# Kernel tuning notes

Measured on AMD Instinct MI355X. Metric: run time of the kernel, lower is better.

## Reference

```python
import jax, jax.numpy as jnp
import numpy as np

NUM_ELEC = 128
TIME_STEPS = 128  # must equal NUM_ELEC for the original module's matmuls to be shape-consistent
NUM_VOXELS = 2052
HIDDEN = 64
DCT_DIM = 512
BATCH = 64
RHO = 0.5
TAU = 0.1
PLV_THRESH = 0.5


def dct_matrix(N, K):
    n = np.arange(N)[None, :]
    k = np.arange(K)[:, None]
    m = np.sqrt(2.0 / N) * np.cos(np.pi * (2 * n + 1) * k / (2 * N))
    m[0, :] = 1.0 / np.sqrt(N)
    return jnp.asarray(m, dtype=jnp.float32)


def setup_inputs() -> dict:
    ks = jax.random.split(jax.random.key(0), 12)
    H = HIDDEN
    return {
        "z": jax.random.normal(ks[0], (BATCH, NUM_ELEC, TIME_STEPS), dtype=jnp.float32),
        "lead_field": jax.random.normal(ks[1], (NUM_VOXELS, NUM_ELEC), dtype=jnp.float32),
        "gumbel_u": jax.random.uniform(ks[2], (NUM_ELEC, NUM_ELEC), dtype=jnp.float32, minval=1e-6, maxval=1.0 - 1e-6),
        "w_gae": jax.random.normal(ks[3], (NUM_ELEC, H), dtype=jnp.float32) / np.sqrt(NUM_ELEC),
        "b_gae": jnp.zeros((H,), dtype=jnp.float32),
        "w1": jax.random.normal(ks[4], (NUM_ELEC, H), dtype=jnp.float32) / np.sqrt(NUM_ELEC),
        "b1": jnp.zeros((H,), dtype=jnp.float32),
        "w2": jax.random.normal(ks[5], (H, H), dtype=jnp.float32) / np.sqrt(H),
        "b2": jnp.zeros((H,), dtype=jnp.float32),
        "w_ih": jax.random.normal(ks[6], (3 * H, H), dtype=jnp.float32) / np.sqrt(H),
        "w_hh": jax.random.normal(ks[7], (3 * H, H), dtype=jnp.float32) / np.sqrt(H),
        "b_ih": jnp.zeros((3 * H,), dtype=jnp.float32),
        "b_hh": jnp.zeros((3 * H,), dtype=jnp.float32),
    }


def _hilbert_phases(z):
    # FFT-based analytic signal along last axis (== scipy.signal.hilbert), then instantaneous phase
    T = z.shape[-1]
    idx = jnp.arange(T)
    hf = jnp.where(idx == 0, 1.0, jnp.where(idx < T // 2, 2.0, jnp.where(idx == T // 2, 1.0, 0.0)))
    analytic = jnp.fft.ifft(jnp.fft.fft(z, axis=-1) * hf, axis=-1)
    return jnp.angle(analytic)


def _forward(z, lead_field, gumbel_u, w_gae, b_gae, w1, b1, w2, b2, w_ih, w_hh, b_ih, b_hh):
    B, N, T = z.shape
    # ---- PLV adjacency: fused broadcast+reduction replacing the 128x128 python double loop ----
    phases = _hilbert_phases(z)                                  # [B,N,T]
    E = jnp.exp(1j * phases).astype(jnp.complex64)
    # plv[i,j] = |mean_{b,t} exp(i(phi_i - phi_j))| = |E_i . conj(E_j)| / (B*T)
    plv = jnp.abs(jnp.einsum('bit,bjt->ij', E, jnp.conj(E))) / (B * T)
    a = (plv >= PLV_THRESH).astype(jnp.float32)                  # [N,N]
    # ---- GAE: GCN encoder on batch-averaged signals + inner-product decoder ----
    x = jnp.mean(z, axis=0)                                      # [N,T] (T == N)
    hg = jax.nn.relu((a @ x) @ w_gae + b_gae)                    # [N,H]
    p = jax.nn.sigmoid(hg @ hg.T)                                # [N,N]
    # ---- Gumbel graph augmentation ----
    e = RHO * p + (1.0 - RHO) * a
    g = -jnp.log(-jnp.log(gumbel_u))
    a_aug = jax.nn.sigmoid((jnp.log(e) - jnp.log(1.0 - e) + g) / TAU)
    # ---- symmetric degree normalization ----
    d_inv_sqrt = jnp.sum(a_aug, axis=-1) ** -0.5
    a_norm = d_inv_sqrt[:, None] * a_aug * d_inv_sqrt[None, :]
    zT = jnp.swapaxes(z, 1, 2)                                   # [B,T,N]
    h = jax.nn.relu(jnp.matmul(a_norm, zT) @ w1 + b1)            # [B,N,H]
    h = jax.nn.relu(jnp.matmul(a_norm, h) @ w2 + b2)             # [B,N,H]
    h_seq = h.reshape(B * T, -1)                                 # [B*T,H]
    # ---- GRU over flattened (B*T) sequence (torch nn.GRU gate order r,z,n) ----
    Hd = w_hh.shape[1]
    def gru_step(hprev, xt):
        gi = xt @ w_ih.T + b_ih
        gh = hprev @ w_hh.T + b_hh
        ir, iz, inn = jnp.split(gi, 3)
        hr, hz, hn = jnp.split(gh, 3)
        r = jax.nn.sigmoid(ir + hr)
        zg = jax.nn.sigmoid(iz + hz)
        cand = jnp.tanh(inn + r * hn)
        hnew = (1.0 - zg) * cand + zg * hprev
        return hnew, hnew
    _, h_gru = jax.lax.scan(gru_step, jnp.zeros((Hd,), z.dtype), h_seq)
    del h_gru  # computed as in the original forward, but not part of the returned tuple
    # ---- lead-field projection + DCT low-pass reconstruction ----
    dct_m = dct_matrix(NUM_VOXELS, DCT_DIM)                      # [K,V]
    s = jnp.matmul(lead_field, zT)                               # [B,V,T]
    s_dct = jnp.matmul(dct_m, s)                                 # [B,K,T]
    s_low = s_dct[:, :DCT_DIM, :]                                # [B,K,T] (full, K == dct_dim)
    s_recon = jnp.matmul(dct_m.T, s_low)                         # [B,V,T]
    return s_low, s_recon, a_aug


def reference(z, lead_field, gumbel_u, w_gae, b_gae, w1, b1, w2, b2, w_ih, w_hh, b_ih, b_hh):
    return _forward(z, lead_field, gumbel_u, w_gae, b_gae, w1, b1, w2, b2, w_ih, w_hh, b_ih, b_hh)
```

## Files before the change

### kernel.cpp

```cpp
#include <hip/hip_runtime.h>

#define NV 2052
#define KD 512
#define RTOT 2564
#define KTOT 256
#define JTOT 8192

typedef __attribute__((ext_vector_type(8))) short short8v;
typedef __attribute__((ext_vector_type(4))) float f32x4;
typedef unsigned short ushort_t;

#define OFF_AF   0u
#define OFF_ABF  65536u
#define OFF_BBF  409600u
#define OFF_YBF  1458176u
#define OFF_PG   2506752u
#define OFF_PM1  6701056u
#define OFF_A    7749632u
#define OFF_X    7766016u
#define OFF_XW   7782400u

#define SREC_OFF 4194304u
#define AAUG_OFF 21004288u

#define GLOAD16(g, l) __builtin_amdgcn_global_load_lds( \
    (const __attribute__((address_space(1))) unsigned int*)(g), \
    (__attribute__((address_space(3))) unsigned int*)(l), 16, 0, 0)

__device__ __forceinline__ float dct_val(int k, int v) {
    if (k == 0) return 1.0f / sqrtf(2052.0f);
    int m = (2 * v + 1) * k;
    int r = m % 8208;
    float ang = (float)((double)r * (3.14159265358979323846 / 4104.0));
    return sqrtf(2.0f / 2052.0f) * cosf(ang);
}

__device__ __forceinline__ void bf16split(float x, ushort_t& hi, ushort_t& lo) {
    unsigned xb = __float_as_uint(x);
    hi = (ushort_t)(xb >> 16);
    float r = x - __uint_as_float((unsigned)hi << 16);
    lo = (ushort_t)(__float_as_uint(r) >> 16);
}

__device__ __forceinline__ ushort_t bf16rn(float x) {
    unsigned xb = __float_as_uint(x);
    return (ushort_t)((xb + 0x7fffu + ((xb >> 16) & 1u)) >> 16);
}

__global__ __launch_bounds__(256) void k_front(const float* __restrict__ LF, const float* __restrict__ z,
                                               float* __restrict__ Pm1,
                                               ushort_t* __restrict__ Ybf, ushort_t* __restrict__ Bbf) {
    __shared__ float sh[8][132];
    const int tid = threadIdx.x;
    const int bid = blockIdx.x;
    if (bid < 1024) {
        const int t = tid & 127;
        const int kk = tid >> 7;
        const int k0 = (bid & 63) * 8;
        const int vch = bid >> 6;
        const int v0 = vch * 128;
        const int nv = (vch == 15) ? 132 : 128;
        for (int p = tid; p < 1056; p += 256) {
            int rr = p / 132, cc = p - rr * 132;
            sh[rr][cc] = dct_val(k0 + rr, v0 + cc);
        }
        __syncthreads();
        const float* lf = LF + (size_t)v0 * 128 + t;
        float a0 = 0.f, a1 = 0.f, a2 = 0.f, a3 = 0.f;
        for (int vi = 0; vi + 2 <= nv; vi += 2) {
            float l0 = lf[vi * 128], l1 = lf[vi * 128 + 128];
            a0 += sh[kk + 0][vi] * l0; a1 += sh[kk + 2][vi] * l0;
            a2 += sh[kk + 4][vi] * l0; a3 += sh[kk + 6][vi] * l0;
            a0 += sh[kk + 0][vi + 1] * l1; a1 += sh[kk + 2][vi + 1] * l1;
            a2 += sh[kk + 4][vi + 1] * l1; a3 += sh[kk + 6][vi + 1] * l1;
        }
        float* P = Pm1 + (size_t)vch * 65536;
        P[(k0 + kk + 0) * 128 + t] = a0;
        P[(k0 + kk + 2) * 128 + t] = a1;
        P[(k0 + kk + 4) * 128 + t] = a2;
        P[(k0 + kk + 6) * 128 + t] = a3;
    } else {
        const int t = tid & 127;
        const int rr = tid >> 7;
        const int rid = (bid - 1024) * 2 + rr;
        const int b = rid >> 7, i = rid & 127;
        sh[rr][t] = z[(size_t)rid * 128 + t];
        if (tid < 128) {
            float hv = 0.f;
            if (t & 1) {
                float ang = 3.14159265358979323846f * (float)t * (1.0f / 128.0f);
                hv = (cosf(ang) / sinf(ang)) * (1.0f / 64.0f);
            }
            sh[2][t] = hv;
        }
        __syncthreads();
        float acc = 0.f;
        #pragma unroll 8
        for (int q = 0; q < 64; ++q) {
            int d = 2 * q + 1;
            acc += sh[2][d] * sh[rr][(t - d) & 127];
        }
        float zv = sh[rr][t];
        float inv = rsqrtf(zv * zv + acc * acc);
        Ybf[(size_t)i * JTOT + b * 128 + t] = bf16rn(zv * inv);
        Ybf[(size_t)(128 + i) * JTOT + b * 128 + t] = bf16rn(acc * inv);
        Bbf[(size_t)rid * 128 + t] = (ushort_t)(__float_as_uint(zv) >> 16);
    }
}

__global__ __launch_bounds__(256) void k_m1red(const float* __restrict__ Pm1, const float* __restrict__ z,
                                               float* __restrict__ AF, ushort_t* __restrict__ Abf,
                                               float* __restrict__ X) {
    const int bid = blockIdx.x;
    if (bid < 256) {
        int id = bid * 256 + threadIdx.x;
        float s = 0.f;
        #pragma unroll
        for (int p = 0; p < 16; ++p) s += Pm1[p * 65536 + id];
        AF[id] = s;
        int rid = id >> 7, t = id & 127;
        ushort_t hi, lo; bf16split(s, hi, lo);
        ushort_t* row = Abf + (size_t)rid * KTOT;
        row[t] = hi; row[128 + t] = lo;
    } else {
        int id = (bid - 256) * 256 + threadIdx.x;
        float s0 = 0.f, s1 = 0.f, s2 = 0.f, s3 = 0.f;
        #pragma unroll 4
        for (int b = 0; b < 64; b += 4) {
            s0 += z[(size_t)(b + 0) * 16384 + id];
            s1 += z[(size_t)(b + 1) * 16384 + id];
            s2 += z[(size_t)(b + 2) * 16384 + id];
            s3 += z[(size_t)(b + 3) * 16384 + id];
        }
        X[id] = ((s0 + s1) + (s2 + s3)) * (1.0f / 64.0f);
    }
}

__global__ __launch_bounds__(256) void k_m2(const float* __restrict__ M1, ushort_t* __restrict__ Abf,
                                            const ushort_t* __restrict__ Ybf, float* __restrict__ Pg) {
    __shared__ float sM1[128][128];
    __shared__ float sdct[8][128];
    const int tid = threadIdx.x;
    const int bid = blockIdx.x;
    if (bid < 257) {
        const int t = tid & 127;
        const int half = tid >> 7;
        const int v0 = bid * 8;
        float acc0 = 0.f, acc1 = 0.f, acc2 = 0.f, acc3 = 0.f;
        for (int kc = 0; kc < KD; kc += 128) {
            __syncthreads();
            #pragma unroll
            for (int q = 0; q < 16; ++q) {
                int f = q * 256 + tid;
                int kr = f >> 5;
                int c4 = (f & 31) * 4;
                *(float4*)&sM1[kr][c4] = *(const float4*)&M1[(size_t)(kc + kr) * 128 + c4];
            }
            #pragma unroll
            for (int p = tid; p < 1024; p += 256)
                sdct[p >> 7][p & 127] = dct_val(kc + (p & 127), v0 + (p >> 7));
            __syncthreads();
            const float* d0 = &sdct[half * 4 + 0][0];
            const float* d1 = &sdct[half * 4 + 1][0];
            const float* d2 = &sdct[half * 4 + 2][0];
            const float* d3 = &sdct[half * 4 + 3][0];
            #pragma unroll 4
            for (int ki = 0; ki < 128; ++ki) {
                float m = sM1[ki][t];
                acc0 += d0[ki] * m;
                acc1 += d1[ki] * m;
                acc2 += d2[ki] * m;
                acc3 += d3[ki] * m;
            }
        }
        float vals[4] = {acc0, acc1, acc2, acc3};
        #pragma unroll
        for (int r = 0; r < 4; ++r) {
            int v = v0 + half * 4 + r;
            if (v < NV) {
                ushort_t hi, lo; bf16split(vals[r], hi, lo);
                ushort_t* row = Abf + (size_t)(KD + v) * KTOT;
                row[t] = hi; row[128 + t] = lo;
            }
        }
    } else {
        const int g = bid - 257;
        const int j0 = (g & 1) * 128;
        const int i0 = ((g >> 1) & 1) * 128;
        const int sk = g >> 2;
        const int kc0 = sk * 256;
        const int wave = tid >> 6;
        const int lane = tid & 63;
        const int wr = wave >> 1, wc = wave & 1;
        const int l15 = lane & 15;
        const int lhi = lane >> 4;
        ushort_t* Al = (ushort_t*)&sM1[0][0];
        ushort_t* Bl = Al + 8192;
        f32x4 acc[4][4];
        #pragma unroll
        for (int i = 0; i < 4; ++i)
            #pragma unroll
            for (int j = 0; j < 4; ++j)
                acc[i][j] = (f32x4){0.f, 0.f, 0.f, 0.f};
        for (int kc = kc0; kc < kc0 + 256; kc += 64) {
            __syncthreads();
            #pragma unroll
            for (int i = 0; i < 4; ++i) {
                int elt = (wave * 4 + i) * 64 + lane;
                int m = elt >> 3;
                int sc = (elt & 7) ^ (m & 7);
                GLOAD16(Ybf + (size_t)(i0 + m) * JTOT + kc + sc * 8, &Al[(wave * 4 + i) * 512]);
                GLOAD16(Ybf + (size_t)(j0 + m) * JTOT + kc + sc * 8, &Bl[(wave * 4 + i) * 512]);
            }
            asm volatile("s_waitcnt vmcnt(0)" ::: "memory");
            __syncthreads();
            #pragma unroll
            for (int kk = 0; kk < 2; ++kk) {
                short8v av[4], bv[4];
                #pragma unroll
                for (int mi = 0; mi < 4; ++mi) {
                    int m = wr * 64 + mi * 16 + l15;
                    int ch = (kk * 4 + lhi) ^ (m & 7);
                    av[mi] = *(const short8v*)&Al[m * 64 + ch * 8];
                }
                #pragma unroll
                for (int ni = 0; ni < 4; ++ni) {
                    int n = wc * 64 + ni * 16 + l15;
                    int ch = (kk * 4 + lhi) ^ (n & 7);
                    bv[ni] = *(const short8v*)&Bl[n * 64 + ch * 8];
                }
                #pragma unroll
                for (int mi = 0; mi < 4; ++mi)
                    #pragma unroll
                    for (int ni = 0; ni < 4; ++ni)
                        acc[mi][ni] = __builtin_amdgcn_mfma_f32_16x16x32_bf16(av[mi], bv[ni], acc[mi][ni], 0, 0, 0);
            }
        }
        const int q = ((g >> 1) & 1) * 2 + (g & 1);
        float* P = Pg + (size_t)(sk * 4 + q) * 16384;
        #pragma unroll
        for (int mi = 0; mi < 4; ++mi)
            #pragma unroll
            for (int reg = 0; reg < 4; ++reg) {
                int rl = wr * 64 + mi * 16 + lhi * 4 + reg;
                #pragma unroll
                for (int ni = 0; ni < 4; ++ni) {
                    int cl = wc * 64 + ni * 16 + l15;
                    P[rl * 128 + cl] = acc[mi][ni][reg];
                }
            }
    }
}

__global__ __launch_bounds__(256) void k_back(const ushort_t* __restrict__ Abf, const ushort_t* __restrict__ Bbf,
                                              float* __restrict__ out, const float* __restrict__ Pg,
                                              const float* __restrict__ X, const float* __restrict__ Wg,
                                              float* __restrict__ A, float* __restrict__ XW) {
    __shared__ ushort_t SM[24576];
    const int tid = threadIdx.x;
    const int bid = blockIdx.x;

    if (bid < 1344) {
        const int wave = tid >> 6;
        const int lane = tid & 63;
        const int wr = wave >> 1, wc = wave & 1;
        const int l15 = lane & 15;
        const int lhi = lane >> 4;
        f32x4 acc[4][4];
        #pragma unroll
        for (int i = 0; i < 4; ++i)
            #pragma unroll
            for (int j = 0; j < 4; ++j)
                acc[i][j] = (f32x4){0.f, 0.f, 0.f, 0.f};
        const int j0 = (bid & 63) * 128;
        const int r0 = (bid >> 6) * 128;
        ushort_t* AlHi = SM;
        ushort_t* AlLo = SM + 8192;
        ushort_t* Bl   = SM + 16384;
        for (int kc = 0; kc < 128; kc += 64) {
            __syncthreads();
            #pragma unroll
            for (int i = 0; i < 4; ++i) {
                int elt = (wave * 4 + i) * 64 + lane;
                int m = elt >> 3;
                int sc = (elt & 7) ^ (m & 7);
                GLOAD16(Abf + (size_t)(r0 + m) * KTOT + kc + sc * 8,       &AlHi[(wave * 4 + i) * 512]);
                GLOAD16(Abf + (size_t)(r0 + m) * KTOT + 128 + kc + sc * 8, &AlLo[(wave * 4 + i) * 512]);
                GLOAD16(Bbf + (size_t)(j0 + m) * 128 + kc + sc * 8,        &Bl[(wave * 4 + i) * 512]);
            }
            asm volatile("s_waitcnt vmcnt(0)" ::: "memory");
            __syncthreads();
            #pragma unroll
            for (int kk = 0; kk < 2; ++kk) {
                short8v ah[4], al[4], bv[4];
                #pragma unroll
                for (int mi = 0; mi < 4; ++mi) {
                    int m = wr * 64 + mi * 16 + l15;
                    int ch = (kk * 4 + lhi) ^ (m & 7);
                    ah[mi] = *(const short8v*)&AlHi[m * 64 + ch * 8];
                    al[mi] = *(const short8v*)&AlLo[m * 64 + ch * 8];
                }
                #pragma unroll
                for (int ni = 0; ni < 4; ++ni) {
                    int n = wc * 64 + ni * 16 + l15;
                    int ch = (kk * 4 + lhi) ^ (n & 7);
                    bv[ni] = *(const short8v*)&Bl[n * 64 + ch * 8];
                }
                #pragma unroll
                for (int mi = 0; mi < 4; ++mi)
                    #pragma unroll
                    for (int ni = 0; ni < 4; ++ni)
                        acc[mi][ni] = __builtin_amdgcn_mfma_f32_16x16x32_bf16(ah[mi], bv[ni], acc[mi][ni], 0, 0, 0);
                #pragma unroll
                for (int mi = 0; mi < 4; ++mi)
                    #pragma unroll
                    for (int ni = 0; ni < 4; ++ni)
                        acc[mi][ni] = __builtin_amdgcn_mfma_f32_16x16x32_bf16(al[mi], bv[ni], acc[mi][ni], 0, 0, 0);
            }
        }
        float* SMf = (float*)SM;
        const unsigned bb = (unsigned)(bid & 63);
        #pragma unroll
        for (int hhalf = 0; hhalf < 2; ++hhalf) {
            __syncthreads();
            if (wc == hhalf) {
                #pragma unroll
                for (int mi = 0; mi < 4; ++mi)
                    #pragma unroll
                    for (int ni = 0; ni < 4; ++ni)
                        #pragma unroll
                        for (int reg = 0; reg < 4; ++reg) {
                            int rl = wr * 64 + mi * 16 + lhi * 4 + reg;
                            int cl = ni * 16 + l15;
                            SMf[rl * 68 + cl] = acc[mi][ni][reg];
                        }
            }
            __syncthreads();
            int rl = tid >> 1;
            int cs = (tid & 1) * 32;
            int r = r0 + rl;
            if (r < RTOT) {
                unsigned base;
                if (r < KD) base = bb * 65536u + (unsigned)r * 128u;
                else        base = SREC_OFF + bb * 262656u + (unsigned)(r - KD) * 128u;
                base += hhalf * 64 + cs;
                const float* src = &SMf[rl * 68 + cs];
                float* dst = out + base;
                #pragma unroll
                for (int q = 0; q < 8; ++q)
                    *(float4*)(dst + q * 4) = *(const float4*)(src + q * 4);
            }
        }
    } else if (bid < 1408) {
        int id = (bid - 1344) * 256 + tid;
        float R = 0.f, I = 0.f;
        #pragma unroll 8
        for (int sk = 0; sk < 32; ++sk) {
            const float* P = Pg + (size_t)sk * 65536 + id;
            R += P[0] + P[3 * 16384];
            I += P[2 * 16384] - P[1 * 16384];
        }
        float plv = sqrtf(R * R + I * I) * (1.0f / 8192.0f);
        A[id] = (plv >= 0.5f) ? 1.0f : 0.0f;
    } else {
        int id = (bid - 1408) * 256 + tid;
        int e = id >> 6, h = id & 63;
        const float* xrow = X + (size_t)e * 128;
        float s = 0.f;
        #pragma unroll 4
        for (int t = 0; t < 128; ++t) s += xrow[t] * Wg[t * 64 + h];
        XW[id] = s;
    }
}

__global__ __launch_bounds__(256) void k_aaugf(const float* __restrict__ A, const float* __restrict__ XW,
                                               const float* __restrict__ bg, const float* __restrict__ U,
                                               float* __restrict__ out) {
    __shared__ float sXW[128][64];
    __shared__ float sHGT[64][128];
    const int tid = threadIdx.x;
    for (int p = tid; p < 8192; p += 256) sXW[p >> 6][p & 63] = XW[p];
    __syncthreads();
    {
        const int r = tid & 127;
        const int half = tid >> 7;
        const float* arow = A + (size_t)r * 128;
        float hacc[32];
        #pragma unroll
        for (int h = 0; h < 32; ++h) hacc[h] = 0.f;
        for (int j = 0; j < 128; ++j) {
            float av = arow[j];
            #pragma unroll
            for (int h = 0; h < 32; ++h) hacc[h] += av * sXW[j][half * 32 + h];
        }
        #pragma unroll
        for (int h = 0; h < 32; ++h)
            sHGT[half * 32 + h][r] = fmaxf(hacc[h] + bg[half * 32 + h], 0.f);
    }
    __syncthreads();
    const int id = blockIdx.x * 256 + tid;
    const int i = id >> 7, j = id & 127;
    float dot = 0.f;
    #pragma unroll 8
    for (int h = 0; h < 64; ++h) dot += sHGT[h][i] * sHGT[h][j];
    float p = 1.f / (1.f + expf(-dot));
    float e = 0.5f * p + 0.5f * A[id];
    float gmb = -logf(-logf(U[id]));
    float arg = (logf(e) - logf(1.f - e) + gmb) * 10.0f;
    out[AAUG_OFF + id] = 1.f / (1.f + expf(-arg));
}

extern "C" void kernel_launch(void* const* d_in, const int* in_sizes, int n_in,
                              void* d_out, int out_size, void* d_ws, size_t ws_size,
                              hipStream_t stream) {
    const float* z  = (const float*)d_in[0];
    const float* LF = (const float*)d_in[1];
    const float* U  = (const float*)d_in[2];
    const float* Wg = (const float*)d_in[3];
    const float* bg = (const float*)d_in[4];
    float* out = (float*)d_out;
    float* W = (float*)d_ws;

    float* AF  = W + OFF_AF;
    ushort_t* Abf = (ushort_t*)(W + OFF_ABF);
    ushort_t* Bbf = (ushort_t*)(W + OFF_BBF);
    ushort_t* Ybf = (ushort_t*)(W + OFF_YBF);
    float* Pg  = W + OFF_PG;
    float* Pm1 = W + OFF_PM1;
    float* A   = W + OFF_A;
    float* X   = W + OFF_X;
    float* XW  = W + OFF_XW;

    k_front<<<5120, 256, 0, stream>>>(LF, z, Pm1, Ybf, Bbf);
    k_m1red<<<320, 256, 0, stream>>>(Pm1, z, AF, Abf, X);
    k_m2   <<<385, 256, 0, stream>>>(AF, Abf, Ybf, Pg);
    k_back <<<1440, 256, 0, stream>>>(Abf, Bbf, out, Pg, X, Wg, A, XW);
    k_aaugf<<<64, 256, 0, stream>>>(A, XW, bg, U, out);
}
```

Baseline: 108.7 us.

## Reschedule work across kernels to merge stages and cut one launch

The PLV Gram GEMM moves from k_m2 into k_m1red. The first four row-tiles of the reconstruction GEMM, which depend only on Abf rows written by k_m1red, move into k_m2. The A_aug computation is folded into k_back as extra blocks, which removes the separate k_aaugf launch and lets independent stages share the GPU. The risk is load imbalance, since k_back's A_aug blocks do a heavy serial dense pass inside a large grid, and it relies on the data dependencies being correctly ordered.

```diff
diff --git a/kernel.cpp b/kernel.cpp
--- a/kernel.cpp
+++ b/kernel.cpp
@@ -45,6 +45,100 @@
 __device__ __forceinline__ ushort_t bf16rn(float x) {
     unsigned xb = __float_as_uint(x);
     return (ushort_t)((xb + 0x7fffu + ((xb >> 16) & 1u)) >> 16);
+}
+
+__device__ __forceinline__ void gemm_tile(ushort_t* SM, const ushort_t* __restrict__ Abf,
+                                          const ushort_t* __restrict__ Bbf, float* __restrict__ out,
+                                          int r0, int jt, int tid) {
+    const int wave = tid >> 6;
+    const int lane = tid & 63;
+    const int wr = wave >> 1, wc = wave & 1;
+    const int l15 = lane & 15;
+    const int lhi = lane >> 4;
+    const int j0 = jt * 128;
+    ushort_t* AlHi = SM;
+    ushort_t* AlLo = SM + 8192;
+    ushort_t* Bl   = SM + 16384;
+    f32x4 acc[4][4];
+    #pragma unroll
+    for (int i = 0; i < 4; ++i)
+        #pragma unroll
+        for (int j = 0; j < 4; ++j)
+            acc[i][j] = (f32x4){0.f, 0.f, 0.f, 0.f};
+    for (int kc = 0; kc < 128; kc += 64) {
+        __syncthreads();
+        #pragma unroll
+        for (int i = 0; i < 4; ++i) {
+            int elt = (wave * 4 + i) * 64 + lane;
+            int m = elt >> 3;
+            int sc = (elt & 7) ^ (m & 7);
+            GLOAD16(Abf + (size_t)(r0 + m) * KTOT + kc + sc * 8,       &AlHi[(wave * 4 + i) * 512]);
+            GLOAD16(Abf + (size_t)(r0 + m) * KTOT + 128 + kc + sc * 8, &AlLo[(wave * 4 + i) * 512]);
+            GLOAD16(Bbf + (size_t)(j0 + m) * 128 + kc + sc * 8,        &Bl[(wave * 4 + i) * 512]);
+        }
+        asm volatile("s_waitcnt vmcnt(0)" ::: "memory");
+        __syncthreads();
+        #pragma unroll
+        for (int kk = 0; kk < 2; ++kk) {
+            short8v ah[4], al[4], bv[4];
+            #pragma unroll
+            for (int mi = 0; mi < 4; ++mi) {
+                int m = wr * 64 + mi * 16 + l15;
+                int ch = (kk * 4 + lhi) ^ (m & 7);
+                ah[mi] = *(const short8v*)&AlHi[m * 64 + ch * 8];
+                al[mi] = *(const short8v*)&AlLo[m * 64 + ch * 8];
+            }
+            #pragma unroll
+            for (int ni = 0; ni < 4; ++ni) {
+                int n = wc * 64 + ni * 16 + l15;
+                int ch = (kk * 4 + lhi) ^ (n & 7);
+                bv[ni] = *(const short8v*)&Bl[n * 64 + ch * 8];
+            }
+            #pragma unroll
+            for (int mi = 0; mi < 4; ++mi)
+                #pragma unroll
+                for (int ni = 0; ni < 4; ++ni)
+                    acc[mi][ni] = __builtin_amdgcn_mfma_f32_16x16x32_bf16(ah[mi], bv[ni], acc[mi][ni], 0, 0, 0);
+            #pragma unroll
+            for (int mi = 0; mi < 4; ++mi)
+                #pragma unroll
+                for (int ni = 0; ni < 4; ++ni)
+                    acc[mi][ni] = __builtin_amdgcn_mfma_f32_16x16x32_bf16(al[mi], bv[ni], acc[mi][ni], 0, 0, 0);
+        }
+    }
+    float* SMf = (float*)SM;
+    const unsigned bb = (unsigned)jt;
+    #pragma unroll
+    for (int hhalf = 0; hhalf < 2; ++hhalf) {
+        __syncthreads();
+        if (wc == hhalf) {
+            #pragma unroll
+            for (int mi = 0; mi < 4; ++mi)
+                #pragma unroll
+                for (int ni = 0; ni < 4; ++ni)
+                    #pragma unroll
+                    for (int reg = 0; reg < 4; ++reg) {
+                        int rl = wr * 64 + mi * 16 + lhi * 4 + reg;
+                        int cl = ni * 16 + l15;
+                        SMf[rl * 68 + cl] = acc[mi][ni][reg];
+                    }
+        }
+        __syncthreads();
+        int rl = tid >> 1;
+        int cs = (tid & 1) * 32;
+        int r = r0 + rl;
+        if (r < RTOT) {
+            unsigned base;
+            if (r < KD) base = bb * 65536u + (unsigned)r * 128u;
+            else        base = SREC_OFF + bb * 262656u + (unsigned)(r - KD) * 128u;
+            base += hhalf * 64 + cs;
+            const float* src = &SMf[rl * 68 + cs];
+            float* dst = out + base;
+            #pragma unroll
+            for (int q = 0; q < 8; ++q)
+                *(float4*)(dst + q * 4) = *(const float4*)(src + q * 4);
+        }
+    }
 }
 
 __global__ __launch_bounds__(256) void k_front(const float* __restrict__ LF, const float* __restrict__ z,
@@ -110,10 +204,13 @@
 
 __global__ __launch_bounds__(256) void k_m1red(const float* __restrict__ Pm1, const float* __restrict__ z,
                                                float* __restrict__ AF, ushort_t* __restrict__ Abf,
-                                               float* __restrict__ X) {
+                                               float* __restrict__ X,
+                                               const ushort_t* __restrict__ Ybf, float* __restrict__ Pg) {
+    __shared__ ushort_t SMg[16384];
+    const int tid = threadIdx.x;
     const int bid = blockIdx.x;
     if (bid < 256) {
-        int id = bid * 256 + threadIdx.x;
+        int id = bid * 256 + tid;
         float s = 0.f;
         #pragma unroll
         for (int p = 0; p < 16; ++p) s += Pm1[p * 65536 + id];
@@ -122,8 +219,8 @@
         ushort_t hi, lo; bf16split(s, hi, lo);
         ushort_t* row = Abf + (size_t)rid * KTOT;
         row[t] = hi; row[128 + t] = lo;
-    } else {
-        int id = (bid - 256) * 256 + threadIdx.x;
+    } else if (bid < 320) {
+        int id = (bid - 256) * 256 + tid;
         float s0 = 0.f, s1 = 0.f, s2 = 0.f, s3 = 0.f;
         #pragma unroll 4
         for (int b = 0; b < 64; b += 4) {
@@ -133,11 +230,80 @@
             s3 += z[(size_t)(b + 3) * 16384 + id];
         }
         X[id] = ((s0 + s1) + (s2 + s3)) * (1.0f / 64.0f);
+    } else {
+        const int g = bid - 320;
+        const int j0 = (g & 1) * 128;
+        const int i0 = ((g >> 1) & 1) * 128;
+        const int sk = g >> 2;
+        const int kc0 = sk * 256;
+        const int wave = tid >> 6;
+        const int lane = tid & 63;
+        const int wr = wave >> 1, wc = wave & 1;
+        const int l15 = lane & 15;
+        const int lhi = lane >> 4;
+        ushort_t* Al = SMg;
+        ushort_t* Bl = SMg + 8192;
+        f32x4 acc[4][4];
+        #pragma unroll
+        for (int i = 0; i < 4; ++i)
+            #pragma unroll
+            for (int j = 0; j < 4; ++j)
+                acc[i][j] = (f32x4){0.f, 0.f, 0.f, 0.f};
+        for (int kc = kc0; kc < kc0 + 256; kc += 64) {
+            __syncthreads();
+            #pragma unroll
+            for (int i = 0; i < 4; ++i) {
+                int elt = (wave * 4 + i) * 64 + lane;
+                int m = elt >> 3;
+                int sc = (elt & 7) ^ (m & 7);
+                GLOAD16(Ybf + (size_t)(i0 + m) * JTOT + kc + sc * 8, &Al[(wave * 4 + i) * 512]);
+                GLOAD16(Ybf + (size_t)(j0 + m) * JTOT + kc + sc * 8, &Bl[(wave * 4 + i) * 512]);
+            }
+            asm volatile("s_waitcnt vmcnt(0)" ::: "memory");
+            __syncthreads();
+            #pragma unroll
+            for (int kk = 0; kk < 2; ++kk) {
+                short8v av[4], bv[4];
+                #pragma unroll
+                for (int mi = 0; mi < 4; ++mi) {
+                    int m = wr * 64 + mi * 16 + l15;
+                    int ch = (kk * 4 + lhi) ^ (m & 7);
+                    av[mi] = *(const short8v*)&Al[m * 64 + ch * 8];
+                }
+                #pragma unroll
+                for (int ni = 0; ni < 4; ++ni) {
+                    int n = wc * 64 + ni * 16 + l15;
+                    int ch = (kk * 4 + lhi) ^ (n & 7);
+                    bv[ni] = *(const short8v*)&Bl[n * 64 + ch * 8];
+                }
+                #pragma unroll
+                for (int mi = 0; mi < 4; ++mi)
+                    #pragma unroll
+                    for (int ni = 0; ni < 4; ++ni)
+                        acc[mi][ni] = __builtin_amdgcn_mfma_f32_16x16x32_bf16(av[mi], bv[ni], acc[mi][ni], 0, 0, 0);
+            }
+        }
+        const int q = ((g >> 1) & 1) * 2 + (g & 1);
+        float* P = Pg + (size_t)(sk * 4 + q) * 16384;
+        #pragma unroll
+        for (int mi = 0; mi < 4; ++mi)
+            #pragma unroll
+            for (int reg = 0; reg < 4; ++reg) {
+                int rl = wr * 64 + mi * 16 + lhi * 4 + reg;
+                #pragma unroll
+                for (int ni = 0; ni < 4; ++ni) {
+                    int cl = wc * 64 + ni * 16 + l15;
+                    P[rl * 128 + cl] = acc[mi][ni][reg];
+                }
+            }
     }
 }
 
 __global__ __launch_bounds__(256) void k_m2(const float* __restrict__ M1, ushort_t* __restrict__ Abf,
-                                            const ushort_t* __restrict__ Ybf, float* __restrict__ Pg) {
+                                            const ushort_t* __restrict__ Bbf, float* __restrict__ out,
+                                            const float* __restrict__ Pg, const float* __restrict__ X,
+                                            const float* __restrict__ Wg,
+                                            float* __restrict__ A, float* __restrict__ XW) {
     __shared__ float sM1[128][128];
     __shared__ float sdct[8][128];
     const int tid = threadIdx.x;
@@ -183,176 +349,11 @@
                 row[t] = hi; row[128 + t] = lo;
             }
         }
-    } else {
+    } else if (bid < 513) {
         const int g = bid - 257;
-        const int j0 = (g & 1) * 128;
-        const int i0 = ((g >> 1) & 1) * 128;
-        const int sk = g >> 2;
-        const int kc0 = sk * 256;
-        const int wave = tid >> 6;
-        const int lane = tid & 63;
-        const int wr = wave >> 1, wc = wave & 1;
-        const int l15 = lane & 15;
-        const int lhi = lane >> 4;
-        ushort_t* Al = (ushort_t*)&sM1[0][0];
-        ushort_t* Bl = Al + 8192;
-        f32x4 acc[4][4];
-        #pragma unroll
-        for (int i = 0; i < 4; ++i)
-            #pragma unroll
-            for (int j = 0; j < 4; ++j)
-                acc[i][j] = (f32x4){0.f, 0.f, 0.f, 0.f};
-        for (int kc = kc0; kc < kc0 + 256; kc += 64) {
-            __syncthreads();
-            #pragma unroll
-            for (int i = 0; i < 4; ++i) {
-                int elt = (wave * 4 + i) * 64 + lane;
-                int m = elt >> 3;
-                int sc = (elt & 7) ^ (m & 7);
-                GLOAD16(Ybf + (size_t)(i0 + m) * JTOT + kc + sc * 8, &Al[(wave * 4 + i) * 512]);
-                GLOAD16(Ybf + (size_t)(j0 + m) * JTOT + kc + sc * 8, &Bl[(wave * 4 + i) * 512]);
-            }
-            asm volatile("s_waitcnt vmcnt(0)" ::: "memory");
-            __syncthreads();
-            #pragma unroll
-            for (int kk = 0; kk < 2; ++kk) {
-                short8v av[4], bv[4];
-                #pragma unroll
-                for (int mi = 0; mi < 4; ++mi) {
-                    int m = wr * 64 + mi * 16 + l15;
-                    int ch = (kk * 4 + lhi) ^ (m & 7);
-                    av[mi] = *(const short8v*)&Al[m * 64 + ch * 8];
-                }
-                #pragma unroll
-                for (int ni = 0; ni < 4; ++ni) {
-                    int n = wc * 64 + ni * 16 + l15;
-                    int ch = (kk * 4 + lhi) ^ (n & 7);
-                    bv[ni] = *(const short8v*)&Bl[n * 64 + ch * 8];
-                }
-                #pragma unroll
-                for (int mi = 0; mi < 4; ++mi)
-                    #pragma unroll
-                    for (int ni = 0; ni < 4; ++ni)
-                        acc[mi][ni] = __builtin_amdgcn_mfma_f32_16x16x32_bf16(av[mi], bv[ni], acc[mi][ni], 0, 0, 0);
-            }
-        }
-        const int q = ((g >> 1) & 1) * 2 + (g & 1);
-        float* P = Pg + (size_t)(sk * 4 + q) * 16384;
-        #pragma unroll
-        for (int mi = 0; mi < 4; ++mi)
-            #pragma unroll
-            for (int reg = 0; reg < 4; ++reg) {
-                int rl = wr * 64 + mi * 16 + lhi * 4 + reg;
-                #pragma unroll
-                for (int ni = 0; ni < 4; ++ni) {
-                    int cl = wc * 64 + ni * 16 + l15;
-                    P[rl * 128 + cl] = acc[mi][ni][reg];
-                }
-            }
-    }
-}
-
-__global__ __launch_bounds__(256) void k_back(const ushort_t* __restrict__ Abf, const ushort_t* __restrict__ Bbf,
-                                              float* __restrict__ out, const float* __restrict__ Pg,
-                                              const float* __restrict__ X, const float* __restrict__ Wg,
-                                              float* __restrict__ A, float* __restrict__ XW) {
-    __shared__ ushort_t SM[24576];
-    const int tid = threadIdx.x;
-    const int bid = blockIdx.x;
-
-    if (bid < 1344) {
-        const int wave = tid >> 6;
-        const int lane = tid & 63;
-        const int wr = wave >> 1, wc = wave & 1;
-        const int l15 = lane & 15;
-        const int lhi = lane >> 4;
-        f32x4 acc[4][4];
-        #pragma unroll
-        for (int i = 0; i < 4; ++i)
-            #pragma unroll
-            for (int j = 0; j < 4; ++j)
-                acc[i][j] = (f32x4){0.f, 0.f, 0.f, 0.f};
-        const int j0 = (bid & 63) * 128;
-        const int r0 = (bid >> 6) * 128;
-        ushort_t* AlHi = SM;
-        ushort_t* AlLo = SM + 8192;
-        ushort_t* Bl   = SM + 16384;
-        for (int kc = 0; kc < 128; kc += 64) {
-            __syncthreads();
-            #pragma unroll
-            for (int i = 0; i < 4; ++i) {
-                int elt = (wave * 4 + i) * 64 + lane;
-                int m = elt >> 3;
-                int sc = (elt & 7) ^ (m & 7);
-                GLOAD16(Abf + (size_t)(r0 + m) * KTOT + kc + sc * 8,       &AlHi[(wave * 4 + i) * 512]);
-                GLOAD16(Abf + (size_t)(r0 + m) * KTOT + 128 + kc + sc * 8, &AlLo[(wave * 4 + i) * 512]);
-                GLOAD16(Bbf + (size_t)(j0 + m) * 128 + kc + sc * 8,        &Bl[(wave * 4 + i) * 512]);
-            }
-            asm volatile("s_waitcnt vmcnt(0)" ::: "memory");
-            __syncthreads();
-            #pragma unroll
-            for (int kk = 0; kk < 2; ++kk) {
-                short8v ah[4], al[4], bv[4];
-                #pragma unroll
-                for (int mi = 0; mi < 4; ++mi) {
-                    int m = wr * 64 + mi * 16 + l15;
-                    int ch = (kk * 4 + lhi) ^ (m & 7);
-                    ah[mi] = *(const short8v*)&AlHi[m * 64 + ch * 8];
-                    al[mi] = *(const short8v*)&AlLo[m * 64 + ch * 8];
-                }
-                #pragma unroll
-                for (int ni = 0; ni < 4; ++ni) {
-                    int n = wc * 64 + ni * 16 + l15;
-                    int ch = (kk * 4 + lhi) ^ (n & 7);
-                    bv[ni] = *(const short8v*)&Bl[n * 64 + ch * 8];
-                }
-                #pragma unroll
-                for (int mi = 0; mi < 4; ++mi)
-                    #pragma unroll
-                    for (int ni = 0; ni < 4; ++ni)
-                        acc[mi][ni] = __builtin_amdgcn_mfma_f32_16x16x32_bf16(ah[mi], bv[ni], acc[mi][ni], 0, 0, 0);
-                #pragma unroll
-                for (int mi = 0; mi < 4; ++mi)
-                    #pragma unroll
-                    for (int ni = 0; ni < 4; ++ni)
-                        acc[mi][ni] = __builtin_amdgcn_mfma_f32_16x16x32_bf16(al[mi], bv[ni], acc[mi][ni], 0, 0, 0);
-            }
-        }
-        float* SMf = (float*)SM;
-        const unsigned bb = (unsigned)(bid & 63);
-        #pragma unroll
-        for (int hhalf = 0; hhalf < 2; ++hhalf) {
-            __syncthreads();
-            if (wc == hhalf) {
-                #pragma unroll
-                for (int mi = 0; mi < 4; ++mi)
-                    #pragma unroll
-                    for (int ni = 0; ni < 4; ++ni)
-                        #pragma unroll
-                        for (int reg = 0; reg < 4; ++reg) {
-                            int rl = wr * 64 + mi * 16 + lhi * 4 + reg;
-                            int cl = ni * 16 + l15;
-                            SMf[rl * 68 + cl] = acc[mi][ni][reg];
-                        }
-            }
-            __syncthreads();
-            int rl = tid >> 1;
-            int cs = (tid & 1) * 32;
-            int r = r0 + rl;
-            if (r < RTOT) {
-                unsigned base;
-                if (r < KD) base = bb * 65536u + (unsigned)r * 128u;
-                else        base = SREC_OFF + bb * 262656u + (unsigned)(r - KD) * 128u;
-                base += hhalf * 64 + cs;
-                const float* src = &SMf[rl * 68 + cs];
-                float* dst = out + base;
-                #pragma unroll
-                for (int q = 0; q < 8; ++q)
-                    *(float4*)(dst + q * 4) = *(const float4*)(src + q * 4);
-            }
-        }
-    } else if (bid < 1408) {
-        int id = (bid - 1344) * 256 + tid;
+        gemm_tile((ushort_t*)&sM1[0][0], Abf, Bbf, out, (g >> 6) * 128, g & 63, tid);
+    } else if (bid < 577) {
+        int id = (bid - 513) * 256 + tid;
         float R = 0.f, I = 0.f;
         #pragma unroll 8
         for (int sk = 0; sk < 32; ++sk) {
@@ -363,7 +364,7 @@
         float plv = sqrtf(R * R + I * I) * (1.0f / 8192.0f);
         A[id] = (plv >= 0.5f) ? 1.0f : 0.0f;
     } else {
-        int id = (bid - 1408) * 256 + tid;
+        int id = (bid - 577) * 256 + tid;
         int e = id >> 6, h = id & 63;
         const float* xrow = X + (size_t)e * 128;
         float s = 0.f;
@@ -373,41 +374,49 @@
     }
 }
 
-__global__ __launch_bounds__(256) void k_aaugf(const float* __restrict__ A, const float* __restrict__ XW,
-                                               const float* __restrict__ bg, const float* __restrict__ U,
-                                               float* __restrict__ out) {
-    __shared__ float sXW[128][64];
-    __shared__ float sHGT[64][128];
+__global__ __launch_bounds__(256) void k_back(const ushort_t* __restrict__ Abf, const ushort_t* __restrict__ Bbf,
+                                              float* __restrict__ out,
+                                              const float* __restrict__ A, const float* __restrict__ XW,
+                                              const float* __restrict__ bg, const float* __restrict__ U) {
+    __shared__ ushort_t SM[24576];
     const int tid = threadIdx.x;
-    for (int p = tid; p < 8192; p += 256) sXW[p >> 6][p & 63] = XW[p];
-    __syncthreads();
-    {
+    const int bid = blockIdx.x;
+    if (bid < 1088) {
+        gemm_tile(SM, Abf, Bbf, out, (4 + (bid >> 6)) * 128, bid & 63, tid);
+    } else {
+        float* sBuf = (float*)SM;
+        const int g = bid - 1088;
+        for (int p = tid; p < 8192; p += 256) sBuf[p] = XW[p];
+        __syncthreads();
+        float hacc[32];
         const int r = tid & 127;
         const int half = tid >> 7;
-        const float* arow = A + (size_t)r * 128;
-        float hacc[32];
-        #pragma unroll
-        for (int h = 0; h < 32; ++h) hacc[h] = 0.f;
-        for (int j = 0; j < 128; ++j) {
-            float av = arow[j];
-            #pragma unroll
-            for (int h = 0; h < 32; ++h) hacc[h] += av * sXW[j][half * 32 + h];
-        }
+        {
+            const float* arow = A + (size_t)r * 128;
+            #pragma unroll
+            for (int h = 0; h < 32; ++h) hacc[h] = 0.f;
+            for (int j = 0; j < 128; ++j) {
+                float av = arow[j];
+                #pragma unroll
+                for (int h = 0; h < 32; ++h) hacc[h] += av * sBuf[j * 64 + half * 32 + h];
+            }
+        }
+        __syncthreads();
         #pragma unroll
         for (int h = 0; h < 32; ++h)
-            sHGT[half * 32 + h][r] = fmaxf(hacc[h] + bg[half * 32 + h], 0.f);
-    }
-    __syncthreads();
-    const int id = blockIdx.x * 256 + tid;
-    const int i = id >> 7, j = id & 127;
-    float dot = 0.f;
-    #pragma unroll 8
-    for (int h = 0; h < 64; ++h) dot += sHGT[h][i] * sHGT[h][j];
-    float p = 1.f / (1.f + expf(-dot));
-    float e = 0.5f * p + 0.5f * A[id];
-    float gmb = -logf(-logf(U[id]));
-    float arg = (logf(e) - logf(1.f - e) + gmb) * 10.0f;
-    out[AAUG_OFF + id] = 1.f / (1.f + expf(-arg));
+            sBuf[(half * 32 + h) * 128 + r] = fmaxf(hacc[h] + bg[half * 32 + h], 0.f);
+        __syncthreads();
+        const int id = g * 256 + tid;
+        const int i = id >> 7, j = id & 127;
+        float dot = 0.f;
+        #pragma unroll 8
+        for (int h = 0; h < 64; ++h) dot += sBuf[h * 128 + i] * sBuf[h * 128 + j];
+        float p = 1.f / (1.f + expf(-dot));
+        float e = 0.5f * p + 0.5f * A[id];
+        float gmb = -logf(-logf(U[id]));
+        float arg = (logf(e) - logf(1.f - e) + gmb) * 10.0f;
+        out[AAUG_OFF + id] = 1.f / (1.f + expf(-arg));
+    }
 }
 
 extern "C" void kernel_launch(void* const* d_in, const int* in_sizes, int n_in,
@@ -432,8 +441,7 @@
     float* XW  = W + OFF_XW;
 
     k_front<<<5120, 256, 0, stream>>>(LF, z, Pm1, Ybf, Bbf);
-    k_m1red<<<320, 256, 0, stream>>>(Pm1, z, AF, Abf, X);
-    k_m2   <<<385, 256, 0, stream>>>(AF, Abf, Ybf, Pg);
-    k_back <<<1440, 256, 0, stream>>>(Abf, Bbf, out, Pg, X, Wg, A, XW);
-    k_aaugf<<<64, 256, 0, stream>>>(A, XW, bg, U, out);
-}
+    k_m1red<<<448, 256, 0, stream>>>(Pm1, z, AF, Abf, X, Ybf, Pg);
+    k_m2   <<<609, 256, 0, stream>>>(AF, Abf, Bbf, out, Pg, X, Wg, A, XW);
+    k_back <<<1152, 256, 0, stream>>>(Abf, Bbf, out, A, XW, bg, U);
+}
```

New measurement: 96.64 us (median of 2 runs). 1.13x faster.
